# Kernel optimization log

Hardware: AMD Instinct MI355X
Metric: run time of the kernel (lower is better)

Reference implementation:

```python
import jax, jax.numpy as jnp
import numpy as np

B, Q, N, K, C = 32, 500, 200, 16, 92
CLASS_COST, POLY_COST, GIOU_COST = 1.0, 5.0, 1.0
EPS = 1e-6


def setup_inputs() -> dict:
    key = jax.random.key(0)
    k1, k2, k3, k4 = jax.random.split(key, 4)
    return {
        "pred_logits": jax.random.normal(k1, (B, Q, C), dtype=jnp.float32),
        "pred_polylines": jax.random.uniform(k2, (B, Q, K, 2), dtype=jnp.float32),
        "tgt_labels": jax.random.randint(k3, (B, N), 0, 91, dtype=jnp.int32),
        "tgt_polylines": jax.random.uniform(k4, (B, N, K, 2), dtype=jnp.float32),
    }


def _poly_to_bbox(p):
    # p: (..., K, 2) -> (..., 4) xyxy
    x, y = p[..., 0], p[..., 1]
    return jnp.stack([x.min(-1), y.min(-1), x.max(-1), y.max(-1)], axis=-1)


def _giou(b1, b2):
    # b1: (B,Q,4), b2: (B,N,4) -> (B,Q,N) pairwise generalized IoU
    area1 = jnp.clip(b1[..., 2] - b1[..., 0], 0) * jnp.clip(b1[..., 3] - b1[..., 1], 0)
    area2 = jnp.clip(b2[..., 2] - b2[..., 0], 0) * jnp.clip(b2[..., 3] - b2[..., 1], 0)
    lt = jnp.maximum(b1[:, :, None, :2], b2[:, None, :, :2])
    rb = jnp.minimum(b1[:, :, None, 2:], b2[:, None, :, 2:])
    wh = jnp.clip(rb - lt, 0)
    inter = wh[..., 0] * wh[..., 1]
    union = area1[:, :, None] + area2[:, None, :] - inter
    iou = inter / jnp.maximum(union, EPS)
    lt_c = jnp.minimum(b1[:, :, None, :2], b2[:, None, :, :2])
    rb_c = jnp.maximum(b1[:, :, None, 2:], b2[:, None, :, 2:])
    wh_c = jnp.clip(rb_c - lt_c, 0)
    area_c = wh_c[..., 0] * wh_c[..., 1]
    return iou - (area_c - union) / jnp.maximum(area_c, EPS)


def reference(pred_logits, pred_polylines, tgt_labels, tgt_polylines):
    # Batched matching cost matrix C: (B, Q, N). The host-side scipy Hungarian
    # solve in the original consumes this matrix; the GPU math being kerneled
    # is exactly this cost computation.
    b, q, k = pred_polylines.shape[0], pred_polylines.shape[1], pred_polylines.shape[2]
    n = tgt_labels.shape[1]
    two_k = 2 * k

    prob = jax.nn.softmax(pred_logits, axis=-1)  # (B,Q,C)
    idx = jnp.broadcast_to(tgt_labels[:, None, :], (b, q, n))
    cost_class = -jnp.take_along_axis(prob, idx, axis=2)  # (B,Q,N)

    out_flat = pred_polylines.reshape(b, q, two_k)
    tgt_flat = tgt_polylines.reshape(b, n, two_k)
    tgt_rev = jnp.flip(tgt_polylines, axis=2).reshape(b, n, two_k)
    # L1 cdist, normalized by 2K; take min over polyline orientation
    cost_fwd = jnp.abs(out_flat[:, :, None, :] - tgt_flat[:, None, :, :]).sum(-1) / float(two_k)
    cost_rev = jnp.abs(out_flat[:, :, None, :] - tgt_rev[:, None, :, :]).sum(-1) / float(two_k)
    cost_poly = jnp.minimum(cost_fwd, cost_rev)

    out_bbox = _poly_to_bbox(pred_polylines)  # (B,Q,4)
    tgt_bbox = _poly_to_bbox(tgt_polylines)   # (B,N,4)
    cost_giou = -_giou(out_bbox, tgt_bbox)    # (B,Q,N)

    return CLASS_COST * cost_class + POLY_COST * cost_poly + GIOU_COST * cost_giou
```

## Files before the change

### kernel.cpp

```cpp
#include <hip/hip_runtime.h>
#include <math.h>

constexpr int B_ = 32, Q_ = 500, N_ = 200, K_ = 16, C_ = 92;
constexpr int TWO_K = 2 * K_;
constexpr int BQ = 16;
constexpr int THREADS = 512;
constexpr int TPAD = 34;
constexpr float CLASS_COST = 1.0f, POLY_COST = 5.0f, GIOU_COST = 1.0f;
constexpr float EPS_ = 1e-6f;

__global__ __launch_bounds__(THREADS)
void matcher_cost_kernel(const float* __restrict__ logits,
                         const float* __restrict__ ppoly,
                         const int*   __restrict__ labels,
                         const float* __restrict__ tpoly,
                         float* __restrict__ out)
{
    __shared__ float sT[N_ * TPAD];
    __shared__ float sTB[N_ * 5];
    __shared__ int   sLbl[N_];
    __shared__ float sProb[BQ * C_];
    __shared__ float sP[BQ * TWO_K];

    const int tid  = threadIdx.x;
    const int qt   = blockIdx.x;
    const int b    = blockIdx.y;
    const int q0   = qt * BQ;
    const int qi   = tid >> 5;
    const int lane = tid & 31;
    const int q    = q0 + qi;
    const bool qvalid = (q < Q_);
    const int nq = min(BQ, Q_ - q0);

    {
        const float* tb_base = tpoly + (size_t)b * (N_ * TWO_K);
        for (int u = tid; u < N_ * TWO_K / 4; u += THREADS) {
            float4 v = reinterpret_cast<const float4*>(tb_base)[u];
            int n = (u * 4) / TWO_K;
            int j = (u * 4) % TWO_K;
            float* d = &sT[n * TPAD + j];
            reinterpret_cast<float2*>(d)[0] = make_float2(v.x, v.y);
            reinterpret_cast<float2*>(d)[1] = make_float2(v.z, v.w);
        }
        for (int n = tid; n < N_; n += THREADS) sLbl[n] = labels[b * N_ + n];

        const float* pp_base = ppoly + ((size_t)(b * Q_ + q0)) * TWO_K;
        for (int u = tid; u < nq * TWO_K; u += THREADS) sP[u] = pp_base[u];

        const float* lg_base = logits + ((size_t)(b * Q_ + q0)) * C_;
        for (int u = tid; u < nq * C_; u += THREADS) sProb[u] = lg_base[u];
    }
    __syncthreads();

    for (int n = tid; n < N_; n += THREADS) {
        const float2* tr = reinterpret_cast<const float2*>(&sT[n * TPAD]);
        float xm = INFINITY, ym = INFINITY, xM = -INFINITY, yM = -INFINITY;
        #pragma unroll
        for (int k = 0; k < K_; ++k) {
            float2 t = tr[k];
            xm = fminf(xm, t.x); xM = fmaxf(xM, t.x);
            ym = fminf(ym, t.y); yM = fmaxf(yM, t.y);
        }
        sTB[n * 5 + 0] = xm; sTB[n * 5 + 1] = ym;
        sTB[n * 5 + 2] = xM; sTB[n * 5 + 3] = yM;
        sTB[n * 5 + 4] = (xM - xm) * (yM - ym);
    }

    {
        float lv[3];
        float m = -INFINITY;
        #pragma unroll
        for (int j = 0; j < 3; ++j) {
            int c = lane + 32 * j;
            lv[j] = (qvalid && c < C_) ? sProb[qi * C_ + c] : -INFINITY;
            m = fmaxf(m, lv[j]);
        }
        #pragma unroll
        for (int off = 16; off; off >>= 1) m = fmaxf(m, __shfl_xor(m, off, 32));
        float s = 0.0f;
        #pragma unroll
        for (int j = 0; j < 3; ++j) {
            int c = lane + 32 * j;
            if (c < C_) { float e = __expf(lv[j] - m); lv[j] = e; s += e; }
        }
        #pragma unroll
        for (int off = 16; off; off >>= 1) s += __shfl_xor(s, off, 32);
        float rs = 1.0f / s;
        if (qvalid) {
            #pragma unroll
            for (int j = 0; j < 3; ++j) {
                int c = lane + 32 * j;
                if (c < C_) sProb[qi * C_ + c] = lv[j] * rs;
            }
        }
    }

    float2 pt[K_];
    float pxm = INFINITY, pym = INFINITY, pxM = -INFINITY, pyM = -INFINITY;
    if (qvalid) {
        const float4* pr = reinterpret_cast<const float4*>(&sP[qi * TWO_K]);
        #pragma unroll
        for (int j = 0; j < 8; ++j) {
            float4 v = pr[j];
            pt[2 * j]     = make_float2(v.x, v.y);
            pt[2 * j + 1] = make_float2(v.z, v.w);
            pxm = fminf(pxm, fminf(v.x, v.z));
            pxM = fmaxf(pxM, fmaxf(v.x, v.z));
            pym = fminf(pym, fminf(v.y, v.w));
            pyM = fmaxf(pyM, fmaxf(v.y, v.w));
        }
    }
    __syncthreads();

    if (!qvalid) return;

    const float parea = (pxM - pxm) * (pyM - pym);
    float* outRow = out + ((size_t)(b * Q_ + q)) * N_;
    const float* probRow = &sProb[qi * C_];

    for (int i = 0; i < 7; ++i) {
        int n = lane + 32 * i;
        if (n >= N_) break;
        const float2* tr = reinterpret_cast<const float2*>(&sT[n * TPAD]);
        float fwd = 0.0f, rev = 0.0f;
        #pragma unroll
        for (int k = 0; k < K_; ++k) {
            float2 t = tr[k];
            float2 pf = pt[k];
            float2 pr = pt[K_ - 1 - k];
            fwd += fabsf(pf.x - t.x) + fabsf(pf.y - t.y);
            rev += fabsf(pr.x - t.x) + fabsf(pr.y - t.y);
        }
        float cpoly = fminf(fwd, rev) * (1.0f / 32.0f);

        float cclass = -probRow[sLbl[n]];

        float tx0 = sTB[n * 5 + 0], ty0 = sTB[n * 5 + 1];
        float tx1 = sTB[n * 5 + 2], ty1 = sTB[n * 5 + 3];
        float tarea = sTB[n * 5 + 4];
        float ix0 = fmaxf(pxm, tx0), iy0 = fmaxf(pym, ty0);
        float ix1 = fminf(pxM, tx1), iy1 = fminf(pyM, ty1);
        float iw = fmaxf(ix1 - ix0, 0.0f), ih = fmaxf(iy1 - iy0, 0.0f);
        float inter = iw * ih;
        float uni = parea + tarea - inter;
        float iou = inter / fmaxf(uni, EPS_);
        float cx0 = fminf(pxm, tx0), cy0 = fminf(pym, ty0);
        float cx1 = fmaxf(pxM, tx1), cy1 = fmaxf(pyM, ty1);
        float cw = fmaxf(cx1 - cx0, 0.0f), ch = fmaxf(cy1 - cy0, 0.0f);
        float ca = cw * ch;
        float giou = iou - (ca - uni) / fmaxf(ca, EPS_);

        outRow[n] = CLASS_COST * cclass + POLY_COST * cpoly - GIOU_COST * giou;
    }
}

extern "C" void kernel_launch(void* const* d_in, const int* in_sizes, int n_in,
                              void* d_out, int out_size, void* d_ws, size_t ws_size,
                              hipStream_t stream) {
    const float* logits = (const float*)d_in[0];
    const float* ppoly  = (const float*)d_in[1];
    const int*   labels = (const int*)d_in[2];
    const float* tpoly  = (const float*)d_in[3];
    float* out = (float*)d_out;

    dim3 grid((Q_ + BQ - 1) / BQ, B_);
    matcher_cost_kernel<<<grid, THREADS, 0, stream>>>(logits, ppoly, labels, tpoly, out);
}
```

Baseline: 26.54 us.

## Map one query per 64-lane wavefront with scalarized pred polyline registers

```diff
diff --git a/kernel.cpp b/kernel.cpp
--- a/kernel.cpp
+++ b/kernel.cpp
@@ -3,13 +3,17 @@
 
 constexpr int B_ = 32, Q_ = 500, N_ = 200, K_ = 16, C_ = 92;
 constexpr int TWO_K = 2 * K_;
-constexpr int BQ = 16;
-constexpr int THREADS = 512;
+constexpr int WAVES = 8;
+constexpr int THREADS = 64 * WAVES;
 constexpr int TPAD = 34;
-constexpr float CLASS_COST = 1.0f, POLY_COST = 5.0f, GIOU_COST = 1.0f;
 constexpr float EPS_ = 1e-6f;
+constexpr float POLY_SCALE = 5.0f / 32.0f;
 
-__global__ __launch_bounds__(THREADS)
+__device__ __forceinline__ float rfl(float v) {
+    return __int_as_float(__builtin_amdgcn_readfirstlane(__float_as_int(v)));
+}
+
+__global__ __launch_bounds__(THREADS, 8)
 void matcher_cost_kernel(const float* __restrict__ logits,
                          const float* __restrict__ ppoly,
                          const int*   __restrict__ labels,
@@ -19,36 +23,26 @@
     __shared__ float sT[N_ * TPAD];
     __shared__ float sTB[N_ * 5];
     __shared__ int   sLbl[N_];
-    __shared__ float sProb[BQ * C_];
-    __shared__ float sP[BQ * TWO_K];
+    __shared__ float sProb[WAVES * C_];
 
     const int tid  = threadIdx.x;
-    const int qt   = blockIdx.x;
     const int b    = blockIdx.y;
-    const int q0   = qt * BQ;
-    const int qi   = tid >> 5;
-    const int lane = tid & 31;
-    const int q    = q0 + qi;
-    const bool qvalid = (q < Q_);
-    const int nq = min(BQ, Q_ - q0);
+    const int q0   = blockIdx.x * WAVES;
+    const int w    = tid >> 6;
+    const int lane = tid & 63;
+    const int q    = q0 + w;
 
     {
         const float* tb_base = tpoly + (size_t)b * (N_ * TWO_K);
         for (int u = tid; u < N_ * TWO_K / 4; u += THREADS) {
             float4 v = reinterpret_cast<const float4*>(tb_base)[u];
-            int n = (u * 4) / TWO_K;
-            int j = (u * 4) % TWO_K;
+            int n = u >> 3;
+            int j = (u & 7) * 4;
             float* d = &sT[n * TPAD + j];
             reinterpret_cast<float2*>(d)[0] = make_float2(v.x, v.y);
             reinterpret_cast<float2*>(d)[1] = make_float2(v.z, v.w);
         }
         for (int n = tid; n < N_; n += THREADS) sLbl[n] = labels[b * N_ + n];
-
-        const float* pp_base = ppoly + ((size_t)(b * Q_ + q0)) * TWO_K;
-        for (int u = tid; u < nq * TWO_K; u += THREADS) sP[u] = pp_base[u];
-
-        const float* lg_base = logits + ((size_t)(b * Q_ + q0)) * C_;
-        for (int u = tid; u < nq * C_; u += THREADS) sProb[u] = lg_base[u];
     }
     __syncthreads();
 
@@ -65,73 +59,64 @@
         sTB[n * 5 + 2] = xM; sTB[n * 5 + 3] = yM;
         sTB[n * 5 + 4] = (xM - xm) * (yM - ym);
     }
+    __syncthreads();
+
+    if (q >= Q_) return;
+
+    const int wq = __builtin_amdgcn_readfirstlane(q);
+    const float* pp = ppoly + ((size_t)(b * Q_ + wq)) * TWO_K;
+    float pfs[TWO_K];
+    #pragma unroll
+    for (int j = 0; j < TWO_K; ++j) pfs[j] = rfl(pp[j]);
+
+    float pxm, pym, pxM, pyM;
+    {
+        float2 p = reinterpret_cast<const float2*>(pp)[lane & 15];
+        float xm = p.x, xM = p.x, ym = p.y, yM = p.y;
+        #pragma unroll
+        for (int off = 8; off; off >>= 1) {
+            xm = fminf(xm, __shfl_xor(xm, off));
+            xM = fmaxf(xM, __shfl_xor(xM, off));
+            ym = fminf(ym, __shfl_xor(ym, off));
+            yM = fmaxf(yM, __shfl_xor(yM, off));
+        }
+        pxm = rfl(xm); pxM = rfl(xM); pym = rfl(ym); pyM = rfl(yM);
+    }
+    const float parea = (pxM - pxm) * (pyM - pym);
 
     {
-        float lv[3];
-        float m = -INFINITY;
+        const float* lg = logits + ((size_t)(b * Q_ + wq)) * C_;
+        float lv0 = lg[lane];
+        float lv1 = (lane < C_ - 64) ? lg[64 + lane] : -INFINITY;
+        float m = fmaxf(lv0, lv1);
         #pragma unroll
-        for (int j = 0; j < 3; ++j) {
-            int c = lane + 32 * j;
-            lv[j] = (qvalid && c < C_) ? sProb[qi * C_ + c] : -INFINITY;
-            m = fmaxf(m, lv[j]);
-        }
+        for (int off = 32; off; off >>= 1) m = fmaxf(m, __shfl_xor(m, off));
+        float e0 = __expf(lv0 - m);
+        float e1 = (lane < C_ - 64) ? __expf(lv1 - m) : 0.0f;
+        float s = e0 + e1;
         #pragma unroll
-        for (int off = 16; off; off >>= 1) m = fmaxf(m, __shfl_xor(m, off, 32));
-        float s = 0.0f;
-        #pragma unroll
-        for (int j = 0; j < 3; ++j) {
-            int c = lane + 32 * j;
-            if (c < C_) { float e = __expf(lv[j] - m); lv[j] = e; s += e; }
-        }
-        #pragma unroll
-        for (int off = 16; off; off >>= 1) s += __shfl_xor(s, off, 32);
+        for (int off = 32; off; off >>= 1) s += __shfl_xor(s, off);
         float rs = 1.0f / s;
-        if (qvalid) {
-            #pragma unroll
-            for (int j = 0; j < 3; ++j) {
-                int c = lane + 32 * j;
-                if (c < C_) sProb[qi * C_ + c] = lv[j] * rs;
-            }
-        }
+        sProb[w * C_ + lane] = e0 * rs;
+        if (lane < C_ - 64) sProb[w * C_ + 64 + lane] = e1 * rs;
     }
 
-    float2 pt[K_];
-    float pxm = INFINITY, pym = INFINITY, pxM = -INFINITY, pyM = -INFINITY;
-    if (qvalid) {
-        const float4* pr = reinterpret_cast<const float4*>(&sP[qi * TWO_K]);
-        #pragma unroll
-        for (int j = 0; j < 8; ++j) {
-            float4 v = pr[j];
-            pt[2 * j]     = make_float2(v.x, v.y);
-            pt[2 * j + 1] = make_float2(v.z, v.w);
-            pxm = fminf(pxm, fminf(v.x, v.z));
-            pxM = fmaxf(pxM, fmaxf(v.x, v.z));
-            pym = fminf(pym, fminf(v.y, v.w));
-            pyM = fmaxf(pyM, fmaxf(v.y, v.w));
-        }
-    }
-    __syncthreads();
+    float* outRow = out + ((size_t)(b * Q_ + wq)) * N_;
+    const float* probRow = &sProb[w * C_];
 
-    if (!qvalid) return;
-
-    const float parea = (pxM - pxm) * (pyM - pym);
-    float* outRow = out + ((size_t)(b * Q_ + q)) * N_;
-    const float* probRow = &sProb[qi * C_];
-
-    for (int i = 0; i < 7; ++i) {
-        int n = lane + 32 * i;
+    for (int i = 0; i < (N_ + 63) / 64; ++i) {
+        int n = lane + 64 * i;
         if (n >= N_) break;
         const float2* tr = reinterpret_cast<const float2*>(&sT[n * TPAD]);
-        float fwd = 0.0f, rev = 0.0f;
+        float f0 = 0.0f, f1 = 0.0f, r0 = 0.0f, r1 = 0.0f;
         #pragma unroll
         for (int k = 0; k < K_; ++k) {
             float2 t = tr[k];
-            float2 pf = pt[k];
-            float2 pr = pt[K_ - 1 - k];
-            fwd += fabsf(pf.x - t.x) + fabsf(pf.y - t.y);
-            rev += fabsf(pr.x - t.x) + fabsf(pr.y - t.y);
+            float a = fabsf(pfs[2 * k]     - t.x) + fabsf(pfs[2 * k + 1] - t.y);
+            float c = fabsf(pfs[30 - 2 * k] - t.x) + fabsf(pfs[31 - 2 * k] - t.y);
+            if (k & 1) { f1 += a; r1 += c; } else { f0 += a; r0 += c; }
         }
-        float cpoly = fminf(fwd, rev) * (1.0f / 32.0f);
+        float cpoly = fminf(f0 + f1, r0 + r1) * POLY_SCALE;
 
         float cclass = -probRow[sLbl[n]];
 
@@ -146,11 +131,10 @@
         float iou = inter / fmaxf(uni, EPS_);
         float cx0 = fminf(pxm, tx0), cy0 = fminf(pym, ty0);
         float cx1 = fmaxf(pxM, tx1), cy1 = fmaxf(pyM, ty1);
-        float cw = fmaxf(cx1 - cx0, 0.0f), ch = fmaxf(cy1 - cy0, 0.0f);
-        float ca = cw * ch;
+        float ca = (cx1 - cx0) * (cy1 - cy0);
         float giou = iou - (ca - uni) / fmaxf(ca, EPS_);
 
-        outRow[n] = CLASS_COST * cclass + POLY_COST * cpoly - GIOU_COST * giou;
+        outRow[n] = cclass + cpoly - giou;
     }
 }
 
@@ -163,6 +147,6 @@
     const float* tpoly  = (const float*)d_in[3];
     float* out = (float*)d_out;
 
-    dim3 grid((Q_ + BQ - 1) / BQ, B_);
+    dim3 grid((Q_ + WAVES - 1) / WAVES, B_);
     matcher_cost_kernel<<<grid, THREADS, 0, stream>>>(logits, ppoly, labels, tpoly, out);
 }
```

Result: slower. 29.27 us (+10.3%).
